# Kernel optimization log

Hardware: AMD Instinct MI355X
Metric: run time of the kernel (lower is better)

The kernel has to match this reference:

```python
import jax, jax.numpy as jnp
import numpy as np

N = 100000
E = 1600000
IN_C = 128
HEADS = 4
HEAD_D = 32  # out_channels(128) // heads(4)


def setup_inputs() -> dict:
    key = jax.random.key(0)
    k1, k2, k3, k4, k5, k6 = jax.random.split(key, 6)
    x = jax.random.normal(k1, (N, IN_C), dtype=jnp.float32)
    edge_index = jax.random.randint(k2, (2, E), 0, N, dtype=jnp.int64)
    edge_weight = jax.random.uniform(k3, (E,), dtype=jnp.float32)
    # params: linear weight stored as [in, H*D] so forward is x @ W (torch does x @ weight.T)
    W = jax.random.normal(k4, (IN_C, HEADS * HEAD_D), dtype=jnp.float32) * (1.0 / np.sqrt(IN_C))
    att_src = jax.random.normal(k5, (HEADS, HEAD_D), dtype=jnp.float32) * 0.1
    att_dst = jax.random.normal(k6, (HEADS, HEAD_D), dtype=jnp.float32) * 0.1
    return {"x": x, "W": W, "att_src": att_src, "att_dst": att_dst,
            "edge_weight": edge_weight, "edge_index": edge_index, "num_nodes": N}


def reference(x, W, att_src, att_dst, edge_weight, edge_index, num_nodes):
    H, D = att_src.shape
    xw = (x @ W).reshape(-1, H, D)                       # [N, H, D]
    row, col = edge_index[0], edge_index[1]
    a_src = jnp.einsum('nhd,hd->nh', xw, att_src)        # [N, H]
    a_dst = jnp.einsum('nhd,hd->nh', xw, att_dst)        # [N, H]
    alpha = jax.nn.leaky_relu(a_src[row] + a_dst[col], negative_slope=0.2)  # [E, H]
    # segment softmax over edges grouped by row (destination of aggregation)
    amax = jax.ops.segment_max(alpha, row, num_segments=num_nodes)          # [N, H]
    amax = jnp.where(jnp.isfinite(amax), amax, 0.0)      # empty segments -> 0 (matches torch init)
    alpha = jnp.exp(alpha - amax[row])
    asum = jax.ops.segment_sum(alpha, row, num_segments=num_nodes)          # [N, H]
    alpha = alpha / (asum[row] + 1e-16)
    msg = xw[col] * alpha[..., None]                     # [E, H, D]
    out = jax.ops.segment_sum(msg, row, num_segments=num_nodes)             # [N, H, D]
    return out.reshape(num_nodes, H * D)
```

## Files before the change

### kernel.cpp

```cpp
#include <hip/hip_runtime.h>
#include <math.h>


typedef _Float16 half4 __attribute__((ext_vector_type(4)));
typedef _Float16 half8 __attribute__((ext_vector_type(8)));
typedef float    f32x4 __attribute__((ext_vector_type(4)));

#define PCHUNK   4096
#define NB_SHIFT 8
#define BCAP     4864

__device__ __forceinline__ float lrelu_exp(float v) {
    v = (v > 0.0f) ? v : 0.2f * v;
    return __expf(v);
}

__global__ __launch_bounds__(256) void k_gemm(const float* __restrict__ x,
                                              const float* __restrict__ W,
                                              const float* __restrict__ att_src,
                                              const float* __restrict__ att_dst,
                                              _Float16* __restrict__ xwh,
                                              float* __restrict__ a_src,
                                              float* __restrict__ a_dst, int N) {
    __shared__ float Ws[32][128];
    __shared__ float xT[32][68];
    int t = threadIdx.x;
    int tx = t & 31;
    int ty = t >> 5;
    int row0 = blockIdx.x * 64;

    float acc[8][4];
    #pragma unroll
    for (int r = 0; r < 8; ++r)
        #pragma unroll
        for (int j = 0; j < 4; ++j) acc[r][j] = 0.f;

    for (int kc = 0; kc < 128; kc += 32) {
        __syncthreads();
        #pragma unroll
        for (int i = 0; i < 4; ++i) {
            int fi = i * 256 + t;
            int kl = fi >> 5, c4 = (fi & 31) << 2;
            *(float4*)&Ws[kl][c4] = *(const float4*)&W[(size_t)(kc + kl) * 128 + c4];
        }
        #pragma unroll
        for (int i = 0; i < 2; ++i) {
            int fi = i * 256 + t;
            int r = fi >> 3, kq = (fi & 7) << 2;
            int grow = row0 + r; if (grow >= N) grow = N - 1;
            float4 v = *(const float4*)&x[(size_t)grow * 128 + kc + kq];
            xT[kq + 0][r] = v.x;
            xT[kq + 1][r] = v.y;
            xT[kq + 2][r] = v.z;
            xT[kq + 3][r] = v.w;
        }
        __syncthreads();
        #pragma unroll 8
        for (int k = 0; k < 32; ++k) {
            float4 wv = *(const float4*)&Ws[k][tx << 2];
            float4 xa = *(const float4*)&xT[k][ty << 3];
            float4 xb = *(const float4*)&xT[k][(ty << 3) + 4];
            float xr[8] = {xa.x, xa.y, xa.z, xa.w, xb.x, xb.y, xb.z, xb.w};
            #pragma unroll
            for (int r = 0; r < 8; ++r) {
                acc[r][0] = fmaf(xr[r], wv.x, acc[r][0]);
                acc[r][1] = fmaf(xr[r], wv.y, acc[r][1]);
                acc[r][2] = fmaf(xr[r], wv.z, acc[r][2]);
                acc[r][3] = fmaf(xr[r], wv.w, acc[r][3]);
            }
        }
    }

    int h  = tx >> 3;
    int dq = (tx & 7) << 2;
    float4 as = *(const float4*)&att_src[h * 32 + dq];
    float4 ad = *(const float4*)&att_dst[h * 32 + dq];
    #pragma unroll
    for (int r = 0; r < 8; ++r) {
        int row = row0 + (ty << 3) + r;
        bool ok = row < N;
        if (ok) {
            half4 hv;
            hv.x = (_Float16)acc[r][0];
            hv.y = (_Float16)acc[r][1];
            hv.z = (_Float16)acc[r][2];
            hv.w = (_Float16)acc[r][3];
            *(half4*)&xwh[(size_t)row * 128 + (tx << 2)] = hv;
        }
        float ps = acc[r][0] * as.x + acc[r][1] * as.y + acc[r][2] * as.z + acc[r][3] * as.w;
        float pd = acc[r][0] * ad.x + acc[r][1] * ad.y + acc[r][2] * ad.z + acc[r][3] * ad.w;
        ps += __shfl_xor(ps, 1); pd += __shfl_xor(pd, 1);
        ps += __shfl_xor(ps, 2); pd += __shfl_xor(pd, 2);
        ps += __shfl_xor(ps, 4); pd += __shfl_xor(pd, 4);
        if (ok && (tx & 7) == 0) {
            a_src[(size_t)row * 4 + h] = ps;
            a_dst[(size_t)row * 4 + h] = pd;
        }
    }
}

__global__ __launch_bounds__(256) void k_part(const int* __restrict__ eidx,
                                              int* __restrict__ bctr,
                                              unsigned long long* __restrict__ rec,
                                              int E) {
    __shared__ unsigned long long buf[PCHUNK];
    __shared__ unsigned long long sbuf[PCHUNK];
    __shared__ int hist[512], excl[512], gbase[512], cur[512];
    __shared__ int wtot[4];
    int t = threadIdx.x;
    int lane = t & 63, wv = t >> 6;
    int e0 = blockIdx.x * PCHUNK;
    int nE = E - e0; if (nE > PCHUNK) nE = PCHUNK;
    hist[t] = 0; hist[t + 256] = 0;
    __syncthreads();
    for (int i = t; i < nE; i += 256) {
        int row = __builtin_nontemporal_load(&eidx[e0 + i]);
        int col = __builtin_nontemporal_load(&eidx[E + e0 + i]);
        buf[i] = ((unsigned long long)(unsigned)col << 32) | (unsigned)row;
        atomicAdd(&hist[row >> NB_SHIFT], 1);
    }
    __syncthreads();
    int h0 = hist[2 * t], h1 = hist[2 * t + 1];
    int s = h0 + h1, sc = s;
    #pragma unroll
    for (int off = 1; off < 64; off <<= 1) {
        int v = __shfl_up(sc, off);
        if (lane >= off) sc += v;
    }
    if (lane == 63) wtot[wv] = sc;
    __syncthreads();
    if (t == 0) {
        int run = 0;
        #pragma unroll
        for (int i = 0; i < 4; ++i) { int tmp = wtot[i]; wtot[i] = run; run += tmp; }
    }
    __syncthreads();
    int incl = sc + wtot[wv];
    excl[2 * t]     = incl - s;
    excl[2 * t + 1] = incl - h1;
    cur[2 * t]      = incl - s;
    cur[2 * t + 1]  = incl - h1;
    gbase[2 * t]     = h0 ? atomicAdd(&bctr[2 * t], h0) : 0;
    gbase[2 * t + 1] = h1 ? atomicAdd(&bctr[2 * t + 1], h1) : 0;
    __syncthreads();
    for (int i = t; i < nE; i += 256) {
        unsigned long long r = buf[i];
        int row = (int)(unsigned)r;
        int dst = atomicAdd(&cur[row >> NB_SHIFT], 1);
        sbuf[dst] = r;
    }
    __syncthreads();
    for (int j = t; j < nE; j += 256) {
        unsigned long long r = sbuf[j];
        int row = (int)(unsigned)r;
        int b = row >> NB_SHIFT;
        int off = gbase[b] + (j - excl[b]);
        if (off < BCAP)
            __builtin_nontemporal_store(r, &rec[(size_t)b * BCAP + off]);
    }
}

__global__ __launch_bounds__(256) void k_csr(const unsigned long long* __restrict__ rec,
                                             const int* __restrict__ bctr,
                                             int* __restrict__ rbeg,
                                             int* __restrict__ rend,
                                             int* __restrict__ csr_col, int N) {
    __shared__ int cnt[256], cur[256];
    __shared__ int wtot[4];
    int b = blockIdx.x;
    int rs = b << NB_SHIFT;
    int t = threadIdx.x;
    int lane = t & 63, wv = t >> 6;
    cnt[t] = 0;
    __syncthreads();
    int m = bctr[b]; if (m > BCAP) m = BCAP;
    const unsigned long long* rr = &rec[(size_t)b * BCAP];
    for (int i = t; i < m; i += 256) {
        int row = (int)(unsigned)rr[i];
        atomicAdd(&cnt[row & 255], 1);
    }
    __syncthreads();
    int c = cnt[t], sc = c;
    #pragma unroll
    for (int off = 1; off < 64; off <<= 1) {
        int v = __shfl_up(sc, off);
        if (lane >= off) sc += v;
    }
    if (lane == 63) wtot[wv] = sc;
    __syncthreads();
    if (t == 0) {
        int run = 0;
        #pragma unroll
        for (int i = 0; i < 4; ++i) { int tmp = wtot[i]; wtot[i] = run; run += tmp; }
    }
    __syncthreads();
    int ex = sc + wtot[wv] - c;
    cur[t] = ex;
    int n = rs + t;
    if (n < N) {
        rbeg[n] = b * BCAP + ex;
        rend[n] = b * BCAP + ex + c;
    }
    __syncthreads();
    for (int i = t; i < m; i += 256) {
        unsigned long long r = rr[i];
        int row = (int)(unsigned)r;
        int col = (int)(r >> 32);
        int slot = atomicAdd(&cur[row & 255], 1);
        csr_col[b * BCAP + slot] = col;
    }
}

__global__ __launch_bounds__(256) void k_agg(const int* __restrict__ rbeg,
                                             const int* __restrict__ rend,
                                             const int* __restrict__ csr_col,
                                             const float* __restrict__ a_src,
                                             const float* __restrict__ a_dst,
                                             const _Float16* __restrict__ xwh,
                                             float* __restrict__ out, int N) {
    int lane = threadIdx.x & 63;
    int n = blockIdx.x * 4 + (threadIdx.x >> 6);
    if (n >= N) return;
    int beg = rbeg[n], end = rend[n];
    int q = lane >> 4;
    int l = lane & 15;
    int h = l >> 2;
    float s_n = a_src[(size_t)n * 4 + h];
    float acc[8] = {0, 0, 0, 0, 0, 0, 0, 0};
    float ws = 0.f;
    int last = end - 1;
    for (int i = beg; i < end; i += 8) {
        int e0 = i + q;
        int e1 = i + 4 + q;
        int e0c = e0 <= last ? e0 : last;
        int e1c = e1 <= last ? e1 : last;
        float m0 = e0 <= last ? 1.f : 0.f;
        float m1 = e1 <= last ? 1.f : 0.f;
        int c0 = __builtin_nontemporal_load(&csr_col[e0c]);
        int c1 = __builtin_nontemporal_load(&csr_col[e1c]);
        float w0 = m0 * lrelu_exp(s_n + a_dst[(size_t)c0 * 4 + h]);
        float w1 = m1 * lrelu_exp(s_n + a_dst[(size_t)c1 * 4 + h]);
        half8 x0 = *(const half8*)&xwh[(size_t)c0 * 128 + (l << 3)];
        half8 x1 = *(const half8*)&xwh[(size_t)c1 * 128 + (l << 3)];
        #pragma unroll
        for (int j = 0; j < 8; ++j)
            acc[j] += w0 * (float)x0[j] + w1 * (float)x1[j];
        ws += w0 + w1;
    }
    #pragma unroll
    for (int j = 0; j < 8; ++j) {
        acc[j] += __shfl_xor(acc[j], 16);
        acc[j] += __shfl_xor(acc[j], 32);
    }
    ws += __shfl_xor(ws, 16);
    ws += __shfl_xor(ws, 32);
    if (q == 0) {
        float inv = 1.0f / (ws + 1e-16f);
        f32x4 o0 = {acc[0] * inv, acc[1] * inv, acc[2] * inv, acc[3] * inv};
        f32x4 o1 = {acc[4] * inv, acc[5] * inv, acc[6] * inv, acc[7] * inv};
        __builtin_nontemporal_store(o0, (f32x4*)&out[(size_t)n * 128 + (l << 3)]);
        __builtin_nontemporal_store(o1, (f32x4*)&out[(size_t)n * 128 + (l << 3) + 4]);
    }
}

extern "C" void kernel_launch(void* const* d_in, const int* in_sizes, int n_in,
                              void* d_out, int out_size, void* d_ws, size_t ws_size,
                              hipStream_t stream) {
    const float* x       = (const float*)d_in[0];
    const float* W       = (const float*)d_in[1];
    const float* att_src = (const float*)d_in[2];
    const float* att_dst = (const float*)d_in[3];
    const int* eidx      = (const int*)d_in[5];
    int N = in_sizes[0] / 128;
    int E = in_sizes[4];
    float* out = (float*)d_out;

    char* p = (char*)d_ws;
    auto alloc = [&](size_t bytes) {
        char* r = p;
        p += (bytes + 255) & ~(size_t)255;
        return r;
    };
    int nbuckets = (N + 255) >> NB_SHIFT;
    _Float16* xwh  = (_Float16*)alloc((size_t)N * 128 * 2);
    float* a_src   = (float*)alloc((size_t)N * 4 * 4);
    float* a_dst   = (float*)alloc((size_t)N * 4 * 4);
    int*   bctr    = (int*)  alloc(512 * 4);
    unsigned long long* rec = (unsigned long long*)alloc((size_t)nbuckets * BCAP * 8);
    int*   rbeg    = (int*)  alloc((size_t)N * 4);
    int*   rend    = (int*)  alloc((size_t)N * 4);
    int*   csr_col = (int*)  alloc((size_t)nbuckets * BCAP * 4);

    (void)hipMemsetAsync(bctr, 0, 512 * 4, stream);
    k_gemm<<<(N + 63) / 64, 256, 0, stream>>>(x, W, att_src, att_dst, xwh, a_src, a_dst, N);
    k_part<<<(E + PCHUNK - 1) / PCHUNK, 256, 0, stream>>>(eidx, bctr, rec, E);
    k_csr<<<nbuckets, 256, 0, stream>>>(rec, bctr, rbeg, rend, csr_col, N);
    k_agg<<<(N + 3) / 4, 256, 0, stream>>>(rbeg, rend, csr_col, a_src, a_dst, xwh, out, N);
}
```

Measured before the change: 271.9 us.

## Batch-load column indices per wave and unroll aggregation over four edges

The aggregation kernel now loads up to 64 CSR column indices in one coalesced wave load and hands them to lanes with shuffles. Each step processes 16 edges, four per quarter-wave, so more gathers of a_dst and xw rows are in flight at once. Row begin/end are packed into one int2 array so each node needs one load instead of two, and leaky-relu is written as fmax. The cost is more registers per thread and a separate masked tail path.

```diff
diff --git a/kernel.cpp b/kernel.cpp
--- a/kernel.cpp
+++ b/kernel.cpp
@@ -11,8 +11,7 @@
 #define BCAP     4864
 
 __device__ __forceinline__ float lrelu_exp(float v) {
-    v = (v > 0.0f) ? v : 0.2f * v;
-    return __expf(v);
+    return __expf(fmaxf(v, 0.2f * v));
 }
 
 __global__ __launch_bounds__(256) void k_gemm(const float* __restrict__ x,
@@ -162,8 +161,7 @@
 
 __global__ __launch_bounds__(256) void k_csr(const unsigned long long* __restrict__ rec,
                                              const int* __restrict__ bctr,
-                                             int* __restrict__ rbeg,
-                                             int* __restrict__ rend,
+                                             int2* __restrict__ rseg,
                                              int* __restrict__ csr_col, int N) {
     __shared__ int cnt[256], cur[256];
     __shared__ int wtot[4];
@@ -198,8 +196,10 @@
     cur[t] = ex;
     int n = rs + t;
     if (n < N) {
-        rbeg[n] = b * BCAP + ex;
-        rend[n] = b * BCAP + ex + c;
+        int2 sg;
+        sg.x = b * BCAP + ex;
+        sg.y = b * BCAP + ex + c;
+        rseg[n] = sg;
     }
     __syncthreads();
     for (int i = t; i < m; i += 256) {
@@ -211,8 +211,7 @@
     }
 }
 
-__global__ __launch_bounds__(256) void k_agg(const int* __restrict__ rbeg,
-                                             const int* __restrict__ rend,
+__global__ __launch_bounds__(256) void k_agg(const int2* __restrict__ rseg,
                                              const int* __restrict__ csr_col,
                                              const float* __restrict__ a_src,
                                              const float* __restrict__ a_dst,
@@ -221,36 +220,65 @@
     int lane = threadIdx.x & 63;
     int n = blockIdx.x * 4 + (threadIdx.x >> 6);
     if (n >= N) return;
-    int beg = rbeg[n], end = rend[n];
+    int2 seg = rseg[n];
+    int beg = seg.x, end = seg.y;
     int q = lane >> 4;
     int l = lane & 15;
     int h = l >> 2;
     float s_n = a_src[(size_t)n * 4 + h];
     float acc[8] = {0, 0, 0, 0, 0, 0, 0, 0};
     float ws = 0.f;
-    int last = end - 1;
-    for (int i = beg; i < end; i += 8) {
-        int e0 = i + q;
-        int e1 = i + 4 + q;
-        int e0c = e0 <= last ? e0 : last;
-        int e1c = e1 <= last ? e1 : last;
-        float m0 = e0 <= last ? 1.f : 0.f;
-        float m1 = e1 <= last ? 1.f : 0.f;
-        int c0 = __builtin_nontemporal_load(&csr_col[e0c]);
-        int c1 = __builtin_nontemporal_load(&csr_col[e1c]);
-        float w0 = m0 * lrelu_exp(s_n + a_dst[(size_t)c0 * 4 + h]);
-        float w1 = m1 * lrelu_exp(s_n + a_dst[(size_t)c1 * 4 + h]);
-        half8 x0 = *(const half8*)&xwh[(size_t)c0 * 128 + (l << 3)];
-        half8 x1 = *(const half8*)&xwh[(size_t)c1 * 128 + (l << 3)];
-        #pragma unroll
-        for (int j = 0; j < 8; ++j)
-            acc[j] += w0 * (float)x0[j] + w1 * (float)x1[j];
-        ws += w0 + w1;
-    }
-    #pragma unroll
-    for (int j = 0; j < 8; ++j) {
-        acc[j] += __shfl_xor(acc[j], 16);
-        acc[j] += __shfl_xor(acc[j], 32);
+
+    for (int w0 = beg; w0 < end; w0 += 64) {
+        int rem = end - w0; if (rem > 64) rem = 64;
+        int cc = (lane < rem) ? __builtin_nontemporal_load(&csr_col[w0 + lane]) : 0;
+        int j = 0;
+        for (; j + 16 <= rem; j += 16) {
+            int c[4]; float ad[4]; half8 xv[4];
+            #pragma unroll
+            for (int u = 0; u < 4; ++u) c[u] = __shfl(cc, j + u * 4 + q);
+            #pragma unroll
+            for (int u = 0; u < 4; ++u) {
+                ad[u] = a_dst[(size_t)c[u] * 4 + h];
+                xv[u] = *(const half8*)&xwh[(size_t)c[u] * 128 + (l << 3)];
+            }
+            #pragma unroll
+            for (int u = 0; u < 4; ++u) {
+                float w = lrelu_exp(s_n + ad[u]);
+                ws += w;
+                #pragma unroll
+                for (int k = 0; k < 8; ++k)
+                    acc[k] += w * (float)xv[u][k];
+            }
+        }
+        if (j < rem) {
+            int c[4]; float m[4]; float ad[4]; half8 xv[4];
+            #pragma unroll
+            for (int u = 0; u < 4; ++u) {
+                int r = j + u * 4 + q;
+                c[u] = __shfl(cc, r);
+                m[u] = (r < rem) ? 1.f : 0.f;
+            }
+            #pragma unroll
+            for (int u = 0; u < 4; ++u) {
+                ad[u] = a_dst[(size_t)c[u] * 4 + h];
+                xv[u] = *(const half8*)&xwh[(size_t)c[u] * 128 + (l << 3)];
+            }
+            #pragma unroll
+            for (int u = 0; u < 4; ++u) {
+                float w = m[u] * lrelu_exp(s_n + ad[u]);
+                ws += w;
+                #pragma unroll
+                for (int k = 0; k < 8; ++k)
+                    acc[k] += w * (float)xv[u][k];
+            }
+        }
+    }
+
+    #pragma unroll
+    for (int k = 0; k < 8; ++k) {
+        acc[k] += __shfl_xor(acc[k], 16);
+        acc[k] += __shfl_xor(acc[k], 32);
     }
     ws += __shfl_xor(ws, 16);
     ws += __shfl_xor(ws, 32);
@@ -287,13 +315,12 @@
     float* a_dst   = (float*)alloc((size_t)N * 4 * 4);
     int*   bctr    = (int*)  alloc(512 * 4);
     unsigned long long* rec = (unsigned long long*)alloc((size_t)nbuckets * BCAP * 8);
-    int*   rbeg    = (int*)  alloc((size_t)N * 4);
-    int*   rend    = (int*)  alloc((size_t)N * 4);
+    int2*  rseg    = (int2*) alloc((size_t)N * 8);
     int*   csr_col = (int*)  alloc((size_t)nbuckets * BCAP * 4);
 
     (void)hipMemsetAsync(bctr, 0, 512 * 4, stream);
     k_gemm<<<(N + 63) / 64, 256, 0, stream>>>(x, W, att_src, att_dst, xwh, a_src, a_dst, N);
     k_part<<<(E + PCHUNK - 1) / PCHUNK, 256, 0, stream>>>(eidx, bctr, rec, E);
-    k_csr<<<nbuckets, 256, 0, stream>>>(rec, bctr, rbeg, rend, csr_col, N);
-    k_agg<<<(N + 3) / 4, 256, 0, stream>>>(rbeg, rend, csr_col, a_src, a_dst, xwh, out, N);
-}
+    k_csr<<<nbuckets, 256, 0, stream>>>(rec, bctr, rseg, csr_col, N);
+    k_agg<<<(N + 3) / 4, 256, 0, stream>>>(rseg, csr_col, a_src, a_dst, xwh, out, N);
+}
```

New measurement: 271.1 us. Within noise of the previous version (-0.3%).
